# Optimization experiments

Measured on AMD Instinct MI355X. Metric: run time of the kernel, lower is better.

## Reference

```python
import jax, jax.numpy as jnp
import numpy as np

DIM = 1024
NUM_HEADS = 16
HEAD_DIM = DIM // NUM_HEADS

def setup_inputs() -> dict:
    key = jax.random.key(0)
    ks = jax.random.split(key, 5)
    s = 1.0 / np.sqrt(DIM)
    x = jax.random.normal(ks[0], (2, 2048, DIM), dtype=jnp.float32)
    W_qkv = jax.random.uniform(ks[1], (DIM, 3 * DIM), dtype=jnp.float32, minval=-s, maxval=s)
    b_qkv = jax.random.uniform(ks[2], (3 * DIM,), dtype=jnp.float32, minval=-s, maxval=s)
    W_out = jax.random.uniform(ks[3], (DIM, DIM), dtype=jnp.float32, minval=-s, maxval=s)
    b_out = jax.random.uniform(ks[4], (DIM,), dtype=jnp.float32, minval=-s, maxval=s)
    return {"x": x, "W_qkv": W_qkv, "b_qkv": b_qkv, "W_out": W_out, "b_out": b_out}

def reference(x, W_qkv, b_qkv, W_out, b_out):
    B, S, _ = x.shape
    qkv = x @ W_qkv + b_qkv                       # [B,S,3*dim]
    q, k, v = jnp.split(qkv, 3, axis=-1)
    # [B,S,dim] -> [B,H,S,hd]
    def to_heads(t):
        return t.reshape(B, S, NUM_HEADS, HEAD_DIM).transpose(0, 2, 1, 3)
    q, k, v = to_heads(q), to_heads(k), to_heads(v)
    scale = HEAD_DIM ** -0.5
    scores = jnp.einsum('bhqd,bhkd->bhqk', q, k) * scale
    attn = jax.nn.softmax(scores, axis=-1)
    out = jnp.einsum('bhqk,bhkd->bhqd', attn, v)  # [B,H,S,hd]
    out = out.transpose(0, 2, 1, 3).reshape(B, S, DIM)
    return out @ W_out + b_out
```

## Files before the change

### kernel.cpp

```cpp
#include <hip/hip_runtime.h>
#include <math.h>

#define DIMM    1024
#define NHEADS  16
#define HDIM    64
#define BATCH   2
#define SEQ     2048
#define ROWS    (BATCH*SEQ)

typedef _Float16 f16x8 __attribute__((ext_vector_type(8)));
typedef _Float16 f16x4 __attribute__((ext_vector_type(4)));
typedef float    f32x4 __attribute__((ext_vector_type(4)));
typedef float    f32x16 __attribute__((ext_vector_type(16)));

__device__ inline void gl_lds16(const void* g, void* l) {
    __builtin_amdgcn_global_load_lds(
        (const __attribute__((address_space(1))) void*)g,
        (__attribute__((address_space(3))) void*)l, 16, 0, 0);
}

static __device__ inline unsigned packh(_Float16 a, _Float16 b) {
    unsigned short ua = __builtin_bit_cast(unsigned short, a);
    unsigned short ub = __builtin_bit_cast(unsigned short, b);
    return (unsigned)ua | ((unsigned)ub << 16);
}
static __device__ inline f16x8 mkfrag(unsigned a, unsigned b, unsigned c, unsigned d) {
    union { unsigned u[4]; f16x8 v; } x;
    x.u[0] = a; x.u[1] = b; x.u[2] = c; x.u[3] = d;
    return x.v;
}

__device__ void tcvt64(const float* __restrict__ in, _Float16* __restrict__ out,
                       int K, int N, int k0, int n0, float (*tile)[65], int t)
{
    {
        const int c4 = (t & 15) * 4;
        const int r  = t >> 4;
        #pragma unroll
        for (int i = 0; i < 4; i++) {
            const int rr = r + 16 * i;
            float4 v = *(const float4*)(in + (size_t)(k0 + rr) * N + n0 + c4);
            tile[rr][c4] = v.x; tile[rr][c4 + 1] = v.y;
            tile[rr][c4 + 2] = v.z; tile[rr][c4 + 3] = v.w;
        }
    }
    __syncthreads();
    #pragma unroll
    for (int i = 0; i < 2; i++) {
        const int seg = t + 256 * i;
        const int n   = seg >> 3;
        const int kc  = (seg & 7) * 8;
        f16x8 o;
        #pragma unroll
        for (int j = 0; j < 8; j++) o[j] = (_Float16)tile[kc + j][n];
        *(f16x8*)(out + (size_t)(n0 + n) * K + k0 + kc) = o;
    }
}

__global__ __launch_bounds__(256)
void prep_kernel(const float* __restrict__ x, const float* __restrict__ Wqkv,
                 const float* __restrict__ Wout, _Float16* __restrict__ xh,
                 _Float16* __restrict__ wqkvt, _Float16* __restrict__ woutt)
{
    __shared__ float tile[64][65];
    const int bx = blockIdx.x;
    const int t  = threadIdx.x;
    if (bx < 2048) {
        const int i = bx * 256 + t;
        const float4 a = *(const float4*)(x + (size_t)i * 8);
        const float4 b = *(const float4*)(x + (size_t)i * 8 + 4);
        f16x8 o;
        o[0] = (_Float16)a.x; o[1] = (_Float16)a.y; o[2] = (_Float16)a.z; o[3] = (_Float16)a.w;
        o[4] = (_Float16)b.x; o[5] = (_Float16)b.y; o[6] = (_Float16)b.z; o[7] = (_Float16)b.w;
        *(f16x8*)(xh + (size_t)i * 8) = o;
    } else if (bx < 2816) {
        const int id = bx - 2048;
        const int gx = id % 48, gy = id / 48;
        tcvt64(Wqkv, wqkvt, DIMM, 3 * DIMM, gy * 64, gx * 64, tile, t);
    } else {
        const int id = bx - 2816;
        const int gx = id & 15, gy = id >> 4;
        tcvt64(Wout, woutt, DIMM, DIMM, gy * 64, gx * 64, tile, t);
    }
}

__global__ __launch_bounds__(256)
void vtranspose_kernel(const _Float16* __restrict__ qkvh, _Float16* __restrict__ vt)
{
    __shared__ _Float16 tile[64][72];
    const int kt = blockIdx.x;
    const int bh = blockIdx.y;
    const int b  = bh >> 4, h = bh & 15;
    const int t  = threadIdx.x;
    {
        const int key = t >> 2, c4 = (t & 3) * 16;
        const _Float16* src = qkvh + ((size_t)(b * SEQ + kt * 64 + key)) * (3 * DIMM)
                              + 2 * DIMM + h * HDIM + c4;
        f16x8 v0 = *(const f16x8*)src;
        f16x8 v1 = *(const f16x8*)(src + 8);
        #pragma unroll
        for (int j = 0; j < 8; j++) {
            tile[c4 + j][key]     = v0[j];
            tile[c4 + 8 + j][key] = v1[j];
        }
    }
    __syncthreads();
    {
        const int d = t >> 2, k4 = (t & 3) * 16;
        f16x8 o0, o1;
        #pragma unroll
        for (int j = 0; j < 8; j++) { o0[j] = tile[d][k4 + j]; o1[j] = tile[d][k4 + 8 + j]; }
        _Float16* dst = vt + ((size_t)bh * 64 + d) * SEQ + kt * 64 + k4;
        *(f16x8*)dst       = o0;
        *(f16x8*)(dst + 8) = o1;
    }
}

template<int OUT_F16>
__global__ __launch_bounds__(256)
void hgemm_bias_kernel(const _Float16* __restrict__ A, const _Float16* __restrict__ Bt,
                       const float* __restrict__ bias, void* __restrict__ Cout,
                       int N, int K)
{
    __shared__ _Float16 As[128 * 64];
    __shared__ _Float16 Bs[128 * 64];

    const int t    = threadIdx.x;
    const int w    = t >> 6, lane = t & 63;
    const int quad = lane >> 4, l16 = lane & 15;
    const int wr   = w >> 1, wc = w & 1;
    const int row0 = blockIdx.y * 128, col0 = blockIdx.x * 128;
    const int sw   = l16 & 7;

    f32x4 acc[4][4];
    #pragma unroll
    for (int i = 0; i < 4; i++)
        #pragma unroll
        for (int j = 0; j < 4; j++)
            #pragma unroll
            for (int r = 0; r < 4; r++) acc[i][j][r] = 0.f;

    const _Float16* gA[4];
    const _Float16* gB[4];
    int lofs[4];
    #pragma unroll
    for (int j = 0; j < 4; j++) {
        const int s   = t + 256 * j;
        const int row = s >> 3;
        const int kb  = (s & 7) ^ (row & 7);
        gA[j] = A  + (size_t)(row0 + row) * K + kb * 8;
        gB[j] = Bt + (size_t)(col0 + row) * K + kb * 8;
        lofs[j] = s * 8;
    }

    const int niter = K >> 6;
    #pragma unroll 1
    for (int it = 0; it < niter; it++) {
        __syncthreads();
        #pragma unroll
        for (int j = 0; j < 4; j++) gl_lds16(gA[j], As + lofs[j]);
        #pragma unroll
        for (int j = 0; j < 4; j++) gl_lds16(gB[j], Bs + lofs[j]);
        #pragma unroll
        for (int j = 0; j < 4; j++) { gA[j] += 64; gB[j] += 64; }
        __syncthreads();

        f16x8 af[4][2], bf[4][2];
        #pragma unroll
        for (int i = 0; i < 4; i++) {
            const int arow = wr * 64 + i * 16 + l16;
            const int brow = wc * 64 + i * 16 + l16;
            #pragma unroll
            for (int hh = 0; hh < 2; hh++) {
                af[i][hh] = *(const f16x8*)(As + (arow * 8 + ((hh * 4 + quad) ^ sw)) * 8);
                bf[i][hh] = *(const f16x8*)(Bs + (brow * 8 + ((hh * 4 + quad) ^ sw)) * 8);
            }
        }
        #pragma unroll
        for (int i = 0; i < 4; i++)
            #pragma unroll
            for (int j = 0; j < 4; j++) {
                acc[i][j] = __builtin_amdgcn_mfma_f32_16x16x32_f16(af[i][0], bf[j][0], acc[i][j], 0, 0, 0);
                acc[i][j] = __builtin_amdgcn_mfma_f32_16x16x32_f16(af[i][1], bf[j][1], acc[i][j], 0, 0, 0);
            }
    }

    #pragma unroll
    for (int j = 0; j < 4; j++) {
        const int col = col0 + wc * 64 + j * 16 + l16;
        const float bv = bias[col];
        #pragma unroll
        for (int i = 0; i < 4; i++) {
            const int row = row0 + wr * 64 + i * 16 + quad * 4;
            #pragma unroll
            for (int r = 0; r < 4; r++) {
                const float v = acc[i][j][r] + bv;
                if (OUT_F16)
                    ((_Float16*)Cout)[(size_t)(row + r) * N + col] = (_Float16)v;
                else
                    ((float*)Cout)[(size_t)(row + r) * N + col] = v;
            }
        }
    }
}

__global__ __launch_bounds__(256, 4)
void flash_attn_kernel(const _Float16* __restrict__ qkv,
                       const _Float16* __restrict__ vtg,
                       _Float16* __restrict__ out)
{
    const int qt = blockIdx.x;
    const int bh = blockIdx.y;
    const int b  = bh >> 4, hd = bh & 15;
    const int t    = threadIdx.x;
    const int w    = t >> 6;
    const int lane = t & 63;
    const int qg   = w >> 1;
    const int kh   = w & 1;
    const int l31  = lane & 31;
    const int hf   = lane >> 5;
    const int l7   = lane & 7;

    __shared__ __align__(16) _Float16 Ks [2][64 * 64];
    __shared__ __align__(16) _Float16 Vts[2][64 * 64];

    const int q0 = qt * 64;
    const size_t rstr = 3 * DIMM;
    const _Float16* qbase = qkv + (size_t)b * SEQ * rstr;

    f16x8 qf[4];
    {
        const _Float16* qrow = qbase + (size_t)(q0 + qg * 32 + l31) * rstr + hd * HDIM;
        #pragma unroll
        for (int dd = 0; dd < 4; dd++)
            qf[dd] = *(const f16x8*)(qrow + dd * 16 + hf * 8);
    }

    f32x16 Oacc[2];
    #pragma unroll
    for (int dh = 0; dh < 2; dh++)
        #pragma unroll
        for (int r = 0; r < 16; r++) Oacc[dh][r] = 0.f;
    float lrow = 0.f;

    const int seg0 = t, seg1 = t + 256;
    const int r0 = seg0 >> 3, lb0 = (seg0 & 7) ^ (r0 & 7);
    const int r1 = seg1 >> 3, lb1 = (seg1 & 7) ^ (r1 & 7);
    const _Float16* gK0 = qbase + (size_t)r0 * rstr + DIMM + hd * HDIM + lb0 * 8;
    const _Float16* gK1 = qbase + (size_t)r1 * rstr + DIMM + hd * HDIM + lb1 * 8;
    const _Float16* gV0 = vtg + ((size_t)bh * 64 + r0) * SEQ + lb0 * 8;
    const _Float16* gV1 = vtg + ((size_t)bh * 64 + r1) * SEQ + lb1 * 8;

    gl_lds16(gK0, &Ks [0][seg0 * 8]);
    gl_lds16(gK1, &Ks [0][seg1 * 8]);
    gl_lds16(gV0, &Vts[0][seg0 * 8]);
    gl_lds16(gV1, &Vts[0][seg1 * 8]);

    #pragma unroll 2
    for (int k0 = 0; k0 < SEQ; k0 += 64) {
        const int cur = (k0 >> 6) & 1;
        const _Float16* KsC  = &Ks [cur][0];
        const _Float16* VtsC = &Vts[cur][0];

        __syncthreads();

        f32x16 sacc;
        #pragma unroll
        for (int r = 0; r < 16; r++) sacc[r] = 0.f;
        #pragma unroll
        for (int dd = 0; dd < 4; dd++) {
            f16x8 kf = *(const f16x8*)(KsC + (kh * 32 + l31) * 64 + (((dd * 2 + hf) ^ l7) * 8));
            sacc = __builtin_amdgcn_mfma_f32_32x32x16_f16(kf, qf[dd], sacc, 0, 0, 0);
        }

        if (k0 + 64 < SEQ) {
            const int nxt = cur ^ 1;
            gl_lds16(gK0 + (size_t)(k0 + 64) * rstr, &Ks [nxt][seg0 * 8]);
            gl_lds16(gK1 + (size_t)(k0 + 64) * rstr, &Ks [nxt][seg1 * 8]);
            gl_lds16(gV0 + (k0 + 64),                &Vts[nxt][seg0 * 8]);
            gl_lds16(gV1 + (k0 + 64),                &Vts[nxt][seg1 * 8]);
        }

        _Float16 hh[16];
        #pragma unroll
        for (int r = 0; r < 16; r++) {
            const float e = __expf(sacc[r] * 0.125f);
            hh[r] = (_Float16)e;
            lrow += (float)hh[r];
        }

        unsigned w01 = packh(hh[0],  hh[1]),  w23 = packh(hh[2],  hh[3]);
        unsigned w45 = packh(hh[4],  hh[5]),  w67 = packh(hh[6],  hh[7]);
        unsigned w89 = packh(hh[8],  hh[9]),  wab = packh(hh[10], hh[11]);
        unsigned wcd = packh(hh[12], hh[13]), wef = packh(hh[14], hh[15]);
        unsigned o01 = __shfl_xor((int)w01, 32), o23 = __shfl_xor((int)w23, 32);
        unsigned o45 = __shfl_xor((int)w45, 32), o67 = __shfl_xor((int)w67, 32);
        unsigned o89 = __shfl_xor((int)w89, 32), oab = __shfl_xor((int)wab, 32);
        unsigned ocd = __shfl_xor((int)wcd, 32), oef = __shfl_xor((int)wef, 32);
        f16x8 pa0 = mkfrag(hf ? o45 : w01, hf ? o67 : w23,
                           hf ? w45 : o01, hf ? w67 : o23);
        f16x8 pa1 = mkfrag(hf ? ocd : w89, hf ? oef : wab,
                           hf ? wcd : o89, hf ? wef : oab);

        #pragma unroll
        for (int dh = 0; dh < 2; dh++) {
            const _Float16* vrow = VtsC + (dh * 32 + l31) * 64;
            f16x8 vf0 = *(const f16x8*)(vrow + (((kh * 4 + 0 + hf) ^ l7) * 8));
            f16x8 vf1 = *(const f16x8*)(vrow + (((kh * 4 + 2 + hf) ^ l7) * 8));
            Oacc[dh] = __builtin_amdgcn_mfma_f32_32x32x16_f16(pa0, vf0, Oacc[dh], 0, 0, 0);
            Oacc[dh] = __builtin_amdgcn_mfma_f32_32x32x16_f16(pa1, vf1, Oacc[dh], 0, 0, 0);
        }
    }

    float lsum = lrow + __shfl_xor(lrow, 32);
    __syncthreads();
    float* Obuf = (float*)&Ks[0][0];
    float* lbuf = (float*)&Vts[0][0];
    if (kh) {
        #pragma unroll
        for (int dh = 0; dh < 2; dh++)
            #pragma unroll
            for (int r = 0; r < 16; r++) {
                const int q = (r & 3) + 8 * (r >> 2) + 4 * hf;
                Obuf[(qg * 32 + q) * 64 + dh * 32 + l31] = Oacc[dh][r];
            }
        if (lane < 32) lbuf[qg * 32 + lane] = lsum;
    }
    __syncthreads();
    if (!kh) {
        const float dnrec = 1.f / (lsum + lbuf[qg * 32 + l31]);
        float dq[16];
        #pragma unroll
        for (int r = 0; r < 16; r++)
            dq[r] = __shfl(dnrec, (r & 3) + 8 * (r >> 2) + 4 * hf);
        #pragma unroll
        for (int dh = 0; dh < 2; dh++)
            #pragma unroll
            for (int r = 0; r < 16; r++) {
                const int q = (r & 3) + 8 * (r >> 2) + 4 * hf;
                const float v = (Oacc[dh][r] + Obuf[(qg * 32 + q) * 64 + dh * 32 + l31])
                                * dq[r];
                out[(size_t)(b * SEQ + q0 + qg * 32 + q) * DIMM + hd * HDIM + dh * 32 + l31] =
                    (_Float16)v;
            }
    }
}

extern "C" void kernel_launch(void* const* d_in, const int* in_sizes, int n_in,
                              void* d_out, int out_size, void* d_ws, size_t ws_size,
                              hipStream_t stream)
{
    const float* x    = (const float*)d_in[0];
    const float* Wqkv = (const float*)d_in[1];
    const float* bqkv = (const float*)d_in[2];
    const float* Wout = (const float*)d_in[3];
    const float* bout = (const float*)d_in[4];
    float* out = (float*)d_out;

    _Float16* qkvh  = (_Float16*)d_ws;
    _Float16* attnh = qkvh  + (size_t)ROWS * 3 * DIMM;
    _Float16* xh    = attnh + (size_t)ROWS * DIMM;
    _Float16* wqkvt = xh    + (size_t)ROWS * DIMM;
    _Float16* woutt = wqkvt + (size_t)3 * DIMM * DIMM;
    _Float16* vtg   = woutt + (size_t)DIMM * DIMM;

    prep_kernel<<<3072, 256, 0, stream>>>(x, Wqkv, Wout, xh, wqkvt, woutt);
    {
        dim3 grid(3 * DIMM / 128, ROWS / 128);
        hgemm_bias_kernel<1><<<grid, 256, 0, stream>>>(xh, wqkvt, bqkv, qkvh, 3 * DIMM, DIMM);
    }
    {
        dim3 grid(SEQ / 64, BATCH * NHEADS);
        vtranspose_kernel<<<grid, 256, 0, stream>>>(qkvh, vtg);
    }
    {
        dim3 grid(SEQ / 64, BATCH * NHEADS);
        flash_attn_kernel<<<grid, 256, 0, stream>>>(qkvh, vtg, attnh);
    }
    {
        dim3 grid(DIMM / 128, ROWS / 128);
        hgemm_bias_kernel<0><<<grid, 256, 0, stream>>>(attnh, woutt, bout, out, DIMM, DIMM);
    }
}
```

Before: 204.7 us.

## Double-buffer LDS in GEMM kernels and use 64-row tiles for output projection

Replaces the single-buffered GEMM with a double-buffered version that issues global-to-LDS loads for the next K tile before computing on the current one, so memory latency can overlap with MFMA work and one barrier per iteration is removed. The tile height becomes a template parameter, and the output projection now uses 64-row tiles to double its grid (256 to 512 blocks) for better CU coverage on the small N=1024 GEMM. LDS usage doubles, which may reduce occupancy. The single barrier before issuing the next loads relies on the async LDS loads completing in time.

Measured after the change: 200.1 us. 2.3% less time.

```diff
diff --git a/kernel.cpp b/kernel.cpp
--- a/kernel.cpp
+++ b/kernel.cpp
@@ -116,68 +116,98 @@
     }
 }
 
-template<int OUT_F16>
+template<int OUT_F16, int BM>
 __global__ __launch_bounds__(256)
-void hgemm_bias_kernel(const _Float16* __restrict__ A, const _Float16* __restrict__ Bt,
-                       const float* __restrict__ bias, void* __restrict__ Cout,
-                       int N, int K)
-{
-    __shared__ _Float16 As[128 * 64];
-    __shared__ _Float16 Bs[128 * 64];
+void hgemm_db_kernel(const _Float16* __restrict__ A, const _Float16* __restrict__ Bt,
+                     const float* __restrict__ bias, void* __restrict__ Cout,
+                     int N, int K)
+{
+    constexpr int MI = BM / 32;
+    __shared__ _Float16 As[2][BM * 64];
+    __shared__ _Float16 Bs[2][128 * 64];
 
     const int t    = threadIdx.x;
     const int w    = t >> 6, lane = t & 63;
     const int quad = lane >> 4, l16 = lane & 15;
     const int wr   = w >> 1, wc = w & 1;
-    const int row0 = blockIdx.y * 128, col0 = blockIdx.x * 128;
+    const int row0 = blockIdx.y * BM, col0 = blockIdx.x * 128;
     const int sw   = l16 & 7;
 
-    f32x4 acc[4][4];
-    #pragma unroll
-    for (int i = 0; i < 4; i++)
+    f32x4 acc[MI][4];
+    #pragma unroll
+    for (int i = 0; i < MI; i++)
         #pragma unroll
         for (int j = 0; j < 4; j++)
             #pragma unroll
             for (int r = 0; r < 4; r++) acc[i][j][r] = 0.f;
 
-    const _Float16* gA[4];
+    const _Float16* gA[MI];
+    int aofs[MI];
+    #pragma unroll
+    for (int j = 0; j < MI; j++) {
+        const int s   = t + 256 * j;
+        const int row = s >> 3;
+        const int kb  = (s & 7) ^ (row & 7);
+        gA[j] = A + (size_t)(row0 + row) * K + kb * 8;
+        aofs[j] = s * 8;
+    }
     const _Float16* gB[4];
-    int lofs[4];
+    int bofs[4];
     #pragma unroll
     for (int j = 0; j < 4; j++) {
         const int s   = t + 256 * j;
         const int row = s >> 3;
         const int kb  = (s & 7) ^ (row & 7);
-        gA[j] = A  + (size_t)(row0 + row) * K + kb * 8;
         gB[j] = Bt + (size_t)(col0 + row) * K + kb * 8;
-        lofs[j] = s * 8;
-    }
+        bofs[j] = s * 8;
+    }
+
+    #pragma unroll
+    for (int j = 0; j < MI; j++) gl_lds16(gA[j], &As[0][aofs[j]]);
+    #pragma unroll
+    for (int j = 0; j < 4; j++)  gl_lds16(gB[j], &Bs[0][bofs[j]]);
+    #pragma unroll
+    for (int j = 0; j < MI; j++) gA[j] += 64;
+    #pragma unroll
+    for (int j = 0; j < 4; j++)  gB[j] += 64;
 
     const int niter = K >> 6;
     #pragma unroll 1
     for (int it = 0; it < niter; it++) {
+        const int cur = it & 1;
         __syncthreads();
-        #pragma unroll
-        for (int j = 0; j < 4; j++) gl_lds16(gA[j], As + lofs[j]);
-        #pragma unroll
-        for (int j = 0; j < 4; j++) gl_lds16(gB[j], Bs + lofs[j]);
-        #pragma unroll
-        for (int j = 0; j < 4; j++) { gA[j] += 64; gB[j] += 64; }
-        __syncthreads();
-
-        f16x8 af[4][2], bf[4][2];
-        #pragma unroll
-        for (int i = 0; i < 4; i++) {
-            const int arow = wr * 64 + i * 16 + l16;
-            const int brow = wc * 64 + i * 16 + l16;
-            #pragma unroll
-            for (int hh = 0; hh < 2; hh++) {
-                af[i][hh] = *(const f16x8*)(As + (arow * 8 + ((hh * 4 + quad) ^ sw)) * 8);
-                bf[i][hh] = *(const f16x8*)(Bs + (brow * 8 + ((hh * 4 + quad) ^ sw)) * 8);
-            }
-        }
-        #pragma unroll
-        for (int i = 0; i < 4; i++)
+
+        if (it + 1 < niter) {
+            const int nxt = cur ^ 1;
+            #pragma unroll
+            for (int j = 0; j < MI; j++) gl_lds16(gA[j], &As[nxt][aofs[j]]);
+            #pragma unroll
+            for (int j = 0; j < 4; j++)  gl_lds16(gB[j], &Bs[nxt][bofs[j]]);
+            #pragma unroll
+            for (int j = 0; j < MI; j++) gA[j] += 64;
+            #pragma unroll
+            for (int j = 0; j < 4; j++)  gB[j] += 64;
+        }
+
+        const _Float16* AsC = &As[cur][0];
+        const _Float16* BsC = &Bs[cur][0];
+        f16x8 af[MI][2], bf[4][2];
+        #pragma unroll
+        for (int i = 0; i < MI; i++) {
+            const int arow = wr * (BM / 2) + i * 16 + l16;
+            #pragma unroll
+            for (int hh = 0; hh < 2; hh++)
+                af[i][hh] = *(const f16x8*)(AsC + (arow * 8 + ((hh * 4 + quad) ^ sw)) * 8);
+        }
+        #pragma unroll
+        for (int j = 0; j < 4; j++) {
+            const int brow = wc * 64 + j * 16 + l16;
+            #pragma unroll
+            for (int hh = 0; hh < 2; hh++)
+                bf[j][hh] = *(const f16x8*)(BsC + (brow * 8 + ((hh * 4 + quad) ^ sw)) * 8);
+        }
+        #pragma unroll
+        for (int i = 0; i < MI; i++)
             #pragma unroll
             for (int j = 0; j < 4; j++) {
                 acc[i][j] = __builtin_amdgcn_mfma_f32_16x16x32_f16(af[i][0], bf[j][0], acc[i][j], 0, 0, 0);
@@ -190,8 +220,8 @@
         const int col = col0 + wc * 64 + j * 16 + l16;
         const float bv = bias[col];
         #pragma unroll
-        for (int i = 0; i < 4; i++) {
-            const int row = row0 + wr * 64 + i * 16 + quad * 4;
+        for (int i = 0; i < MI; i++) {
+            const int row = row0 + wr * (BM / 2) + i * 16 + quad * 4;
             #pragma unroll
             for (int r = 0; r < 4; r++) {
                 const float v = acc[i][j][r] + bv;
@@ -367,7 +397,7 @@
     prep_kernel<<<3072, 256, 0, stream>>>(x, Wqkv, Wout, xh, wqkvt, woutt);
     {
         dim3 grid(3 * DIMM / 128, ROWS / 128);
-        hgemm_bias_kernel<1><<<grid, 256, 0, stream>>>(xh, wqkvt, bqkv, qkvh, 3 * DIMM, DIMM);
+        hgemm_db_kernel<1, 128><<<grid, 256, 0, stream>>>(xh, wqkvt, bqkv, qkvh, 3 * DIMM, DIMM);
     }
     {
         dim3 grid(SEQ / 64, BATCH * NHEADS);
@@ -378,7 +408,7 @@
         flash_attn_kernel<<<grid, 256, 0, stream>>>(qkvh, vtg, attnh);
     }
     {
-        dim3 grid(DIMM / 128, ROWS / 128);
-        hgemm_bias_kernel<0><<<grid, 256, 0, stream>>>(attnh, woutt, bout, out, DIMM, DIMM);
-    }
-}
+        dim3 grid(DIMM / 128, ROWS / 64);
+        hgemm_db_kernel<0, 64><<<grid, 256, 0, stream>>>(attnh, woutt, bout, out, DIMM, DIMM);
+    }
+}
```
